# Performance work log

Hardware: AMD Instinct MI355X
Metric: run time of the kernel (lower is better)

## Reference

```python
import jax, jax.numpy as jnp
import numpy as np

B, S, D_MODEL = 1, 1024, 1024
D_CKV, D_CQ = 256, 512
N_HEAD, D_HEAD, D_ROPE = 8, 64, 32


def setup_inputs() -> dict:
    key = jax.random.key(0)
    ks = jax.random.split(key, 12)
    def w(k, shape):
        return jax.random.normal(k, shape, dtype=jnp.float32) * 0.02
    return {
        "x": jax.random.normal(ks[0], (B, S, D_MODEL), dtype=jnp.float32),
        "w_q_idx": w(ks[1], (D_MODEL, N_HEAD * D_HEAD)),
        "w_k_idx": w(ks[2], (D_MODEL, D_HEAD)),
        "w_idx": jnp.ones((N_HEAD,), dtype=jnp.float32),
        "raw_delta": jnp.zeros((D_ROPE // 2,), dtype=jnp.float32),
        "w_dkv": w(ks[3], (D_MODEL, D_CKV)),
        "w_uk": w(ks[4], (D_CKV, N_HEAD * D_HEAD)),
        "w_uv": w(ks[5], (D_CKV, N_HEAD * D_HEAD)),
        "w_dq": w(ks[6], (D_MODEL, D_CQ)),
        "w_uq": w(ks[7], (D_CQ, N_HEAD * D_HEAD)),
        "w_qr": w(ks[8], (D_CQ, N_HEAD * D_ROPE)),
        "w_kr": w(ks[9], (D_MODEL, D_ROPE)),
        "w_out": w(ks[10], (N_HEAD * D_HEAD, D_MODEL)),
        "k_ts": 128,
        "local_window": 64,
    }


def _pope(x, raw_delta, theta):
    # x: (b, L, H, d_rope); positions run along axis 1 (matches torch PoPE)
    delta = -2.0 * jnp.pi * jax.nn.sigmoid(raw_delta)            # (d2,)
    pos = jnp.arange(x.shape[1], dtype=x.dtype)
    ang = pos[None, :, None, None] * theta + delta               # (1, L, 1, d2)
    c, s = jnp.cos(ang), jnp.sin(ang)
    mu1, mu2 = jnp.split(jax.nn.softplus(x), 2, axis=-1)
    return jnp.concatenate((mu1 * c - mu2 * s, mu1 * s + mu2 * c), axis=-1)


def reference(x, w_q_idx, w_k_idx, w_idx, raw_delta, w_dkv, w_uk, w_uv,
              w_dq, w_uq, w_qr, w_kr, w_out, k_ts, local_window):
    b, s, _ = x.shape
    h, dh, dr = N_HEAD, D_HEAD, D_ROPE
    theta = 1.0 / (10000.0 ** (2.0 * jnp.arange(dr // 2, dtype=jnp.float32) / dr))

    # ---- LightningIndexer: per-head relu'd relevance, combined with learned head weights
    qI = (x @ w_q_idx).reshape(b, s, h, dh)
    kI = x @ w_k_idx                                             # (b, s, dh)
    sc = jax.nn.relu(jnp.einsum('bthd,bsd->bths', qI, kI))
    I = jnp.einsum('bths,h->bts', sc, w_idx)

    # ---- TokenSelector: force local window in, mask future out, top-k indices
    qp = jnp.arange(s)[:, None]
    kp = jnp.arange(s)[None, :]
    local = (kp >= qp - local_window + 1) & (kp <= qp)
    causal = kp > qp
    I = jnp.where(local, jnp.inf, I)
    I = jnp.where(causal, -jnp.inf, I)
    k = min(k_ts, s)
    _, idx = jax.lax.top_k(I, k)                                 # (b, s, k) int32

    gather = jax.vmap(lambda t, i: t[i])                         # (s,d),(l,k)->(l,k,d)

    # ---- MLA latent KV, gathered per query
    c_kv = x @ w_dkv                                             # (b, s, d_ckv)
    ckv_sel = gather(c_kv, idx)                                  # (b, s, k, d_ckv)
    key_c = (ckv_sel @ w_uk).reshape(b, s, k, h, dh).transpose(0, 3, 1, 2, 4)
    value = (ckv_sel @ w_uv).reshape(b, s, k, h, dh).transpose(0, 3, 1, 2, 4)

    c_q = x @ w_dq
    query_c = (c_q @ w_uq).reshape(b, s, h, dh).transpose(0, 2, 1, 3)
    query_r = _pope((c_q @ w_qr).reshape(b, s, h, dr), raw_delta, theta).transpose(0, 2, 1, 3)

    # key rope: PoPE applied with positions along the k (selected-token) axis,
    # exactly as the torch code's permute(0,2,1,3) does
    x_sel = gather(x, idx)                                       # (b, s, k, d_model)
    kr = _pope((x_sel @ w_kr).transpose(0, 2, 1, 3), raw_delta, theta).transpose(0, 2, 1, 3)
    key_r = jnp.broadcast_to(kr[:, None], (b, h, s, k, dr))

    query = jnp.concatenate((query_c, query_r), axis=-1)         # (b, h, s, dh+dr)
    keyt = jnp.concatenate((key_c, key_r), axis=-1)              # (b, h, s, k, dh+dr)
    scale = (dh + dr) ** -0.5
    scores = jnp.einsum('bhld,bhlkd->bhlk', query, keyt) * scale
    attn = jax.nn.softmax(scores, axis=-1)
    out = jnp.einsum('bhlk,bhlkd->bhld', attn, value)
    out = out.transpose(0, 2, 1, 3).reshape(b, s, h * dh)
    return out @ w_out
```

## Files before the change

kernel.cpp:

```cpp
#include <hip/hip_runtime.h>
#include <math.h>

#define S_LEN 1024
#define NH 8

typedef __attribute__((ext_vector_type(8))) short bf16x8;
typedef __attribute__((ext_vector_type(4))) float f32x4;

__device__ __forceinline__ float sp_softplus(float x) {
    return fmaxf(x, 0.f) + log1pf(expf(-fabsf(x)));
}

__device__ __forceinline__ unsigned short bfu(float f) {
    unsigned u = __float_as_uint(f);
    unsigned r = (u + 0x7FFFu + ((u >> 16) & 1u)) >> 16;
    return (unsigned short)r;
}

struct FRONT {
    const float *x, *wqidx, *wkidx, *raw_delta, *wuk;
    const float *wdkv, *wdq, *wkr, *wuq, *wqr, *wuv, *wout;
    float *qIP, *kIP, *csc, *css;
    unsigned short *wdkvT, *wdqT, *wkrT, *wuqT, *wqrT, *wuvT, *woutT, *wukb;
};

__global__ __launch_bounds__(256) void front_kernel(FRONT f)
{
    __shared__ float As[2][16][18];
    __shared__ float Bs[2][16][68];
    __shared__ unsigned short tile[64][65];
    int bx = blockIdx.x;
    if (bx < 1152) {
        int gx = bx % 18, gy = bx / 18;
        int half = threadIdx.x >> 7;
        int t = threadIdx.x & 127;
        int u = gx * 2 + half;
        const float* B; float* C;
        int ldb, N, n0, kb;
        if (u < 32) {
            B = f.wqidx; ldb = 512; N = 512;
            C = f.qIP + (long)(u >> 3) * 524288;
            n0 = (u & 7) * 64;
            kb = (u >> 3) * 256;
        } else {
            B = f.wkidx; ldb = 64; N = 64;
            C = f.kIP + (long)(u - 32) * 65536;
            n0 = 0;
            kb = (u - 32) * 256;
        }
        int ke = kb + 256;
        int m0 = gy * 16;
        int ar = t >> 2, ak = t & 3;
        int bk = t >> 3, bn = t & 7;
        int ty = t >> 4, tx = t & 15;

        float4 aN = make_float4(0.f, 0.f, 0.f, 0.f);
        if (t < 64) aN = *(const float4*)(f.x + (long)(m0 + ar) * 1024 + kb + ak * 4);
        float4 b0 = *(const float4*)(B + (long)(kb + bk) * ldb + n0 + bn * 4);
        float4 b1 = *(const float4*)(B + (long)(kb + bk) * ldb + n0 + (bn + 8) * 4);
        float acc[2][4] = {};
        for (int k0 = kb; k0 < ke; k0 += 16) {
            if (t < 64) {
                As[half][ak * 4 + 0][ar] = aN.x;
                As[half][ak * 4 + 1][ar] = aN.y;
                As[half][ak * 4 + 2][ar] = aN.z;
                As[half][ak * 4 + 3][ar] = aN.w;
            }
            *(float4*)&Bs[half][bk][bn * 4] = b0;
            *(float4*)&Bs[half][bk][(bn + 8) * 4] = b1;
            __syncthreads();
            if (k0 + 16 < ke) {
                if (t < 64) aN = *(const float4*)(f.x + (long)(m0 + ar) * 1024 + (k0 + 16) + ak * 4);
                b0 = *(const float4*)(B + (long)(k0 + 16 + bk) * ldb + n0 + bn * 4);
                b1 = *(const float4*)(B + (long)(k0 + 16 + bk) * ldb + n0 + (bn + 8) * 4);
            }
            #pragma unroll
            for (int kk = 0; kk < 16; ++kk) {
                float2 a = *(float2*)&As[half][kk][ty * 2];
                float4 b = *(float4*)&Bs[half][kk][tx * 4];
                acc[0][0] += a.x * b.x; acc[0][1] += a.x * b.y;
                acc[0][2] += a.x * b.z; acc[0][3] += a.x * b.w;
                acc[1][0] += a.y * b.x; acc[1][1] += a.y * b.y;
                acc[1][2] += a.y * b.z; acc[1][3] += a.y * b.w;
            }
            __syncthreads();
        }
        #pragma unroll
        for (int i = 0; i < 2; ++i) {
            float4 v = make_float4(acc[i][0], acc[i][1], acc[i][2], acc[i][3]);
            *(float4*)(C + (long)(m0 + ty * 2 + i) * N + n0 + tx * 4) = v;
        }
    } else if (bx < 1616) {
        int b = bx - 1152;
        const float* srcs[7] = {f.wdkv, f.wdq, f.wkr, f.wuq, f.wqr, f.wuv, f.wout};
        unsigned short* dsts[7] = {f.wdkvT, f.wdqT, f.wkrT, f.wuqT, f.wqrT, f.wuvT, f.woutT};
        const int Ns[7]   = {256, 512, 32, 512, 256, 512, 1024};
        const int Klds[7] = {1024, 1024, 1024, 512, 512, 256, 512};
        const int Ntl[7]  = {4, 8, 1, 8, 4, 8, 16};
        const int bst[8]  = {0, 64, 192, 208, 272, 304, 336, 464};
        int e = 0;
        #pragma unroll
        for (int i = 1; i < 7; ++i) if (b >= bst[i]) e = i;
        int lb = b - bst[e];
        int nt = lb % Ntl[e], kt = lb / Ntl[e];
        const float* src = srcs[e];
        unsigned short* dst = dsts[e];
        int N = Ns[e], Kld = Klds[e];
        int k0 = kt * 64, n0 = nt * 64;
        int t = threadIdx.x;
        int c = t & 63, r4 = t >> 6;
        #pragma unroll
        for (int it = 0; it < 16; ++it) {
            int r = it * 4 + r4;
            float v = (n0 + c < N) ? src[(long)(k0 + r) * N + n0 + c] : 0.f;
            tile[r][c] = bfu(v);
        }
        __syncthreads();
        int wq = t & 7;
        #pragma unroll
        for (int itw = 0; itw < 2; ++itw) {
            int wr = itw * 32 + (t >> 3);
            if (n0 + wr < N) {
                unsigned short v[8];
                #pragma unroll
                for (int j = 0; j < 8; ++j) v[j] = tile[wq * 8 + j][wr];
                *(uint4*)(dst + (long)(n0 + wr) * Kld + k0 + wq * 8) = *(uint4*)v;
            }
        }
    } else if (bx < 1624) {
        int idx = (bx - 1616) * 256 + threadIdx.x;
        int j = idx >> 4, i = idx & 15;
        float rd = f.raw_delta[i];
        float delta = -6.283185307179586f * (1.f / (1.f + expf(-rd)));
        float th = exp2f(-(float)i * 0.83048202372184f);
        float ang = (float)j * th + delta;
        float sv, cv;
        sincosf(ang, &sv, &cv);
        f.csc[idx] = cv;
        f.css[idx] = sv;
    } else {
        int idx = (bx - 1624) * 256 + threadIdx.x;
        f.wukb[idx] = bfu(f.wuk[idx]);
    }
}

struct MFG {
    const float* A[10]; const unsigned short* B[10]; float* C[10];
    int lda[10], ldb[10], ldc[10], K[10], N[10], obf[10];
    int tstart[11]; int ne;
};

__global__ __launch_bounds__(256) void mgemm(MFG mg)
{
    int bx = blockIdx.x, e = 0;
    #pragma unroll
    for (int i = 1; i < 10; ++i) if (i < mg.ne && bx >= mg.tstart[i]) e = i;
    const float* A = mg.A[e];
    const unsigned short* B = mg.B[e];
    float* C = mg.C[e];
    int lda = mg.lda[e], ldb = mg.ldb[e], ldc = mg.ldc[e];
    int K = mg.K[e], N = mg.N[e];
    int m0 = blockIdx.y * 64, n0 = (bx - mg.tstart[e]) * 64;

    __shared__ unsigned short As[64][40];
    __shared__ unsigned short Bs[64][40];
    int t = threadIdx.x;
    int srow = t >> 2, skq = t & 3;
    int wid = t >> 6, l = t & 63;
    int wm = (wid >> 1) * 32, wn = (wid & 1) * 32;
    int fr = l & 15, fk = (l >> 4) * 8;
    bool bok = (n0 + srow) < N;

    f32x4 acc00 = {0.f, 0.f, 0.f, 0.f};
    f32x4 acc01 = {0.f, 0.f, 0.f, 0.f};
    f32x4 acc10 = {0.f, 0.f, 0.f, 0.f};
    f32x4 acc11 = {0.f, 0.f, 0.f, 0.f};

    for (int k0 = 0; k0 < K; k0 += 32) {
        {
            const float* ap = A + (long)(m0 + srow) * lda + k0 + skq * 8;
            float4 v0 = *(const float4*)ap;
            float4 v1 = *(const float4*)(ap + 4);
            unsigned short* d = &As[srow][skq * 8];
            d[0] = bfu(v0.x); d[1] = bfu(v0.y); d[2] = bfu(v0.z); d[3] = bfu(v0.w);
            d[4] = bfu(v1.x); d[5] = bfu(v1.y); d[6] = bfu(v1.z); d[7] = bfu(v1.w);
        }
        {
            uint4 bv = make_uint4(0u, 0u, 0u, 0u);
            if (bok) bv = *(const uint4*)(B + (long)(n0 + srow) * ldb + k0 + skq * 8);
            *(uint4*)&Bs[srow][skq * 8] = bv;
        }
        __syncthreads();
        bf16x8 a0 = *(bf16x8*)&As[wm + fr][fk];
        bf16x8 a1 = *(bf16x8*)&As[wm + 16 + fr][fk];
        bf16x8 b0 = *(bf16x8*)&Bs[wn + fr][fk];
        bf16x8 b1 = *(bf16x8*)&Bs[wn + 16 + fr][fk];
        acc00 = __builtin_amdgcn_mfma_f32_16x16x32_bf16(a0, b0, acc00, 0, 0, 0);
        acc01 = __builtin_amdgcn_mfma_f32_16x16x32_bf16(a0, b1, acc01, 0, 0, 0);
        acc10 = __builtin_amdgcn_mfma_f32_16x16x32_bf16(a1, b0, acc10, 0, 0, 0);
        acc11 = __builtin_amdgcn_mfma_f32_16x16x32_bf16(a1, b1, acc11, 0, 0, 0);
        __syncthreads();
    }
    int crow = (l >> 4) * 4;
    int col0 = n0 + wn + fr, col1 = n0 + wn + 16 + fr;
    if (mg.obf[e]) {
        unsigned short* Cu = (unsigned short*)C;
        if (col0 < N) {
            #pragma unroll
            for (int r = 0; r < 4; ++r) {
                Cu[(long)(m0 + wm + crow + r) * ldc + col0]      = bfu(acc00[r]);
                Cu[(long)(m0 + wm + 16 + crow + r) * ldc + col0] = bfu(acc10[r]);
            }
        }
        if (col1 < N) {
            #pragma unroll
            for (int r = 0; r < 4; ++r) {
                Cu[(long)(m0 + wm + crow + r) * ldc + col1]      = bfu(acc01[r]);
                Cu[(long)(m0 + wm + 16 + crow + r) * ldc + col1] = bfu(acc11[r]);
            }
        }
    } else {
        if (col0 < N) {
            #pragma unroll
            for (int r = 0; r < 4; ++r) {
                C[(long)(m0 + wm + crow + r) * ldc + col0]      = acc00[r];
                C[(long)(m0 + wm + 16 + crow + r) * ldc + col0] = acc10[r];
            }
        }
        if (col1 < N) {
            #pragma unroll
            for (int r = 0; r < 4; ++r) {
                C[(long)(m0 + wm + crow + r) * ldc + col1]      = acc01[r];
                C[(long)(m0 + wm + 16 + crow + r) * ldc + col1] = acc11[r];
            }
        }
    }
}

struct MIDARG {
    const float *qIP, *kIP, *w_idx; float* I;
    const float* qc; const unsigned short* wukb; float* qabs;
    const float *qrp, *raw_delta; float* qrr;
    const float* xkr; float* mu;
};

__global__ __launch_bounds__(256) void mid_kernel(MIDARG g)
{
    __shared__ __align__(16) char smem[26112];
    int b = blockIdx.x;
    int t = threadIdx.x;
    if (b < 512) {
        int sb = b % 16, tb = b / 16;
        if (sb * 64 > tb * 32 + 31) return;
        int t0 = tb * 32, s0 = sb * 64;
        float (*ksT)[68] = (float(*)[68])smem;
        float (*qs)[68]  = (float(*)[68])(smem + 17408);
        {
            int r = t & 63, q = t >> 6;
            #pragma unroll
            for (int u = 0; u < 4; ++u) {
                int c4 = q * 4 + u;
                long off = (long)(s0 + r) * 64 + c4 * 4;
                float4 v = *(const float4*)(g.kIP + off);
                #pragma unroll
                for (int s = 1; s < 4; ++s) {
                    float4 v2 = *(const float4*)(g.kIP + (long)s * 65536 + off);
                    v.x += v2.x; v.y += v2.y; v.z += v2.z; v.w += v2.w;
                }
                ksT[c4 * 4 + 0][r] = v.x;
                ksT[c4 * 4 + 1][r] = v.y;
                ksT[c4 * 4 + 2][r] = v.z;
                ksT[c4 * 4 + 3][r] = v.w;
            }
        }
        int ty = t >> 4, tx = t & 15;
        float accI[2][4] = {};
        for (int h = 0; h < 8; ++h) {
            __syncthreads();
            {
                int r = t >> 3, q = t & 7;
                long base = (long)(t0 + r) * 512 + h * 64;
                #pragma unroll
                for (int half = 0; half < 2; ++half) {
                    long off = base + (q + half * 8) * 4;
                    float4 a = *(const float4*)(g.qIP + off);
                    #pragma unroll
                    for (int s = 1; s < 4; ++s) {
                        float4 a1 = *(const float4*)(g.qIP + (long)s * 524288 + off);
                        a.x += a1.x; a.y += a1.y; a.z += a1.z; a.w += a1.w;
                    }
                    *(float4*)&qs[r][(q + half * 8) * 4] = a;
                }
            }
            __syncthreads();
            float acc[2][4] = {};
            #pragma unroll
            for (int dc = 0; dc < 4; ++dc) {
                float a0[16], a1[16];
                #pragma unroll
                for (int u = 0; u < 4; ++u) {
                    float4 v0 = *(float4*)&qs[ty * 2][dc * 16 + u * 4];
                    float4 v1 = *(float4*)&qs[ty * 2 + 1][dc * 16 + u * 4];
                    a0[u * 4 + 0] = v0.x; a0[u * 4 + 1] = v0.y; a0[u * 4 + 2] = v0.z; a0[u * 4 + 3] = v0.w;
                    a1[u * 4 + 0] = v1.x; a1[u * 4 + 1] = v1.y; a1[u * 4 + 2] = v1.z; a1[u * 4 + 3] = v1.w;
                }
                #pragma unroll
                for (int kk = 0; kk < 16; ++kk) {
                    int d = dc * 16 + kk;
                    float4 bb = *(float4*)&ksT[d][tx * 4];
                    acc[0][0] += a0[kk] * bb.x; acc[0][1] += a0[kk] * bb.y;
                    acc[0][2] += a0[kk] * bb.z; acc[0][3] += a0[kk] * bb.w;
                    acc[1][0] += a1[kk] * bb.x; acc[1][1] += a1[kk] * bb.y;
                    acc[1][2] += a1[kk] * bb.z; acc[1][3] += a1[kk] * bb.w;
                }
            }
            float wh = g.w_idx[h];
            #pragma unroll
            for (int i = 0; i < 2; ++i)
                #pragma unroll
                for (int j = 0; j < 4; ++j)
                    accI[i][j] += wh * fmaxf(acc[i][j], 0.f);
        }
        #pragma unroll
        for (int i = 0; i < 2; ++i) {
            float4 v = make_float4(accI[i][0], accI[i][1], accI[i][2], accI[i][3]);
            *(float4*)&g.I[(long)(t0 + ty * 2 + i) * 1024 + s0 + tx * 4] = v;
        }
    } else if (b < 1024) {
        int lb = b - 512;
        int h = lb >> 6, rem = lb & 63;
        int n0 = (rem >> 4) * 64, m0 = (rem & 15) * 64;
        const float* A = g.qc + h * 64;
        const unsigned short* B = g.wukb + h * 64;
        float* C = g.qabs + h * 256;
        unsigned short (*As)[40] = (unsigned short(*)[40])smem;
        unsigned short (*Bs)[40] = (unsigned short(*)[40])(smem + 5120);
        int srow = t >> 2, skq = t & 3;
        int wid = t >> 6, l = t & 63;
        int wm = (wid >> 1) * 32, wn = (wid & 1) * 32;
        int fr = l & 15, fk = (l >> 4) * 8;
        f32x4 acc00 = {0.f, 0.f, 0.f, 0.f};
        f32x4 acc01 = {0.f, 0.f, 0.f, 0.f};
        f32x4 acc10 = {0.f, 0.f, 0.f, 0.f};
        f32x4 acc11 = {0.f, 0.f, 0.f, 0.f};
        for (int k0 = 0; k0 < 64; k0 += 32) {
            {
                const float* ap = A + (long)(m0 + srow) * 512 + k0 + skq * 8;
                float4 v0 = *(const float4*)ap;
                float4 v1 = *(const float4*)(ap + 4);
                unsigned short* d = &As[srow][skq * 8];
                d[0] = bfu(v0.x); d[1] = bfu(v0.y); d[2] = bfu(v0.z); d[3] = bfu(v0.w);
                d[4] = bfu(v1.x); d[5] = bfu(v1.y); d[6] = bfu(v1.z); d[7] = bfu(v1.w);
            }
            {
                uint4 bv = *(const uint4*)(B + (long)(n0 + srow) * 512 + k0 + skq * 8);
                *(uint4*)&Bs[srow][skq * 8] = bv;
            }
            __syncthreads();
            bf16x8 a0 = *(bf16x8*)&As[wm + fr][fk];
            bf16x8 a1 = *(bf16x8*)&As[wm + 16 + fr][fk];
            bf16x8 b0 = *(bf16x8*)&Bs[wn + fr][fk];
            bf16x8 b1 = *(bf16x8*)&Bs[wn + 16 + fr][fk];
            acc00 = __builtin_amdgcn_mfma_f32_16x16x32_bf16(a0, b0, acc00, 0, 0, 0);
            acc01 = __builtin_amdgcn_mfma_f32_16x16x32_bf16(a0, b1, acc01, 0, 0, 0);
            acc10 = __builtin_amdgcn_mfma_f32_16x16x32_bf16(a1, b0, acc10, 0, 0, 0);
            acc11 = __builtin_amdgcn_mfma_f32_16x16x32_bf16(a1, b1, acc11, 0, 0, 0);
            __syncthreads();
        }
        int crow = (l >> 4) * 4;
        int col0 = n0 + wn + fr, col1 = n0 + wn + 16 + fr;
        #pragma unroll
        for (int r = 0; r < 4; ++r) {
            C[(long)(m0 + wm + crow + r) * 2048 + col0]      = acc00[r];
            C[(long)(m0 + wm + 16 + crow + r) * 2048 + col0] = acc10[r];
            C[(long)(m0 + wm + crow + r) * 2048 + col1]      = acc01[r];
            C[(long)(m0 + wm + 16 + crow + r) * 2048 + col1] = acc11[r];
        }
    } else if (b < 1536) {
        int tq = (b - 1024) * 2 + (t >> 7);
        int tt = t & 127;
        int h = tt >> 4, i = tt & 15;
        float rd = g.raw_delta[i];
        float delta = -6.283185307179586f * (1.f / (1.f + expf(-rd)));
        float th = exp2f(-(float)i * 0.83048202372184f);
        float ang = (float)tq * th + delta;
        float sv, cv;
        sincosf(ang, &sv, &cv);
        float m1 = sp_softplus(g.qrp[tq * 256 + h * 32 + i]);
        float m2 = sp_softplus(g.qrp[tq * 256 + h * 32 + 16 + i]);
        g.qrr[tq * 256 + h * 32 + i]      = m1 * cv - m2 * sv;
        g.qrr[tq * 256 + h * 32 + 16 + i] = m1 * sv + m2 * cv;
    } else {
        int i = (b - 1536) * 256 + t;
        g.mu[i] = sp_softplus(g.xkr[i]);
    }
}

__global__ __launch_bounds__(256) void topk_kernel(
    const float* __restrict__ I, int* __restrict__ idxout)
{
    int t = blockIdx.x * 4 + (threadIdx.x >> 6);
    int lane = threadIdx.x & 63;
    int smin = max(0, t - 63);
    int w = min(64, t + 1);
    if (lane < w) idxout[t * 128 + lane] = smin + lane;
    for (int q = t + 1 + lane; q < 128; q += 64)
        idxout[t * 128 + q] = q;
    int f = max(0, t - 63);
    int m = min(f, 64);
    if (m == 0) return;
    const float* row = I + (long)t * 1024;

    unsigned long long key[16];
    #pragma unroll
    for (int g4 = 0; g4 < 4; ++g4) {
        float4 v = *(const float4*)(row + lane * 16 + g4 * 4);
        float vv[4] = {v.x, v.y, v.z, v.w};
        #pragma unroll
        for (int j = 0; j < 4; ++j) {
            int s = lane * 16 + g4 * 4 + j;
            unsigned long long k = 0ull;
            if (s < f) {
                unsigned u = __float_as_uint(vv[j]);
                unsigned ou = (u & 0x80000000u) ? ~u : (u | 0x80000000u);
                k = ((unsigned long long)ou << 32) | (0xFFFFFFFFu - (unsigned)s);
            }
            key[g4 * 4 + j] = k;
        }
    }

    #pragma unroll
    for (int km = 1; km <= 10; ++km) {
        #pragma unroll
        for (int jm = km - 1; jm >= 0; --jm) {
            if (jm >= 4) {
                int lmask = 1 << (jm - 4);
                #pragma unroll
                for (int r = 0; r < 16; ++r) {
                    unsigned long long other = __shfl_xor(key[r], lmask, 64);
                    int i = lane * 16 + r;
                    bool keep_max = (((i & (1 << km)) == 0) == ((i & (1 << jm)) == 0));
                    unsigned long long mx = key[r] > other ? key[r] : other;
                    unsigned long long mn = key[r] > other ? other : key[r];
                    key[r] = keep_max ? mx : mn;
                }
            } else {
                int rmask = 1 << jm;
                #pragma unroll
                for (int r = 0; r < 16; ++r) {
                    if ((r & rmask) == 0) {
                        int r2 = r | rmask;
                        int i = lane * 16 + r;
                        bool keep_max_low = ((i & (1 << km)) == 0);
                        unsigned long long a = key[r], b = key[r2];
                        unsigned long long mx = a > b ? a : b;
                        unsigned long long mn = a > b ? b : a;
                        key[r]  = keep_max_low ? mx : mn;
                        key[r2] = keep_max_low ? mn : mx;
                    }
                }
            }
        }
    }

    if (lane < 4) {
        #pragma unroll
        for (int r = 0; r < 16; ++r) {
            int e = lane * 16 + r;
            if (e < m) {
                int s = (int)(0xFFFFFFFFu - (unsigned)(key[r] & 0xFFFFFFFFull));
                idxout[t * 128 + w + e] = s;
            }
        }
    }
}

__global__ __launch_bounds__(256) void attn_kernel(
    const float* __restrict__ qabs, const float* __restrict__ qrr,
    const unsigned short* __restrict__ ckvb, const float* __restrict__ mu,
    const float* __restrict__ csc, const float* __restrict__ css,
    const int* __restrict__ idxb, float* __restrict__ olat)
{
    __shared__ unsigned short kv[64][296];
    __shared__ float sc[8][68];
    __shared__ float hs[16];
    __shared__ int idx_s[128];

    int t = blockIdx.x, tid = threadIdx.x;
    int w = tid >> 6, l = tid & 63;
    const float scale = 0.10206207261596575f;

    if (tid < 128) idx_s[tid] = idxb[t * 128 + tid];
    {
        int r = tid >> 5;
        for (int c = tid & 31; c < 296; c += 32) {
            float v = 0.f;
            if (c < 256)      v = qabs[(long)t * 2048 + r * 256 + c] * scale;
            else if (c < 288) v = qrr[(long)t * 256 + r * 32 + (c - 256)] * scale;
            kv[r][c] = bfu(v);
            kv[r + 8][c] = 0;
        }
    }
    __syncthreads();

    bf16x8 qf[9];
    #pragma unroll
    for (int ks = 0; ks < 9; ++ks)
        qf[ks] = *(bf16x8*)&kv[l & 15][ks * 32 + (l >> 4) * 8];

    float mrun0 = -INFINITY, mrun1 = -INFINITY;
    float lrun0 = 0.f, lrun1 = 0.f;
    float acc0 = 0, acc1 = 0, acc2 = 0, acc3 = 0;
    float acc4 = 0, acc5 = 0, acc6 = 0, acc7 = 0;

    int sr = tid >> 2, sq = tid & 3;
    int hpv = l >> 3;
    int c8 = w * 64 + (l & 7) * 8;

    #pragma unroll
    for (int chunk = 0; chunk < 2; ++chunk) {
        __syncthreads();
        {
            int src = idx_s[chunk * 64 + sr];
            const uint4* sp = (const uint4*)(ckvb + (long)src * 256) + sq * 8;
            uint4* dp = (uint4*)&kv[sr][0] + sq * 8;
            #pragma unroll
            for (int g = 0; g < 8; ++g) dp[g] = sp[g];
        }
        {
            int src = idx_s[chunk * 64 + sr];
            int j = chunk * 64 + sr;
            unsigned short hh[8];
            #pragma unroll
            for (int ii = 0; ii < 8; ++ii) {
                int i = sq * 8 + ii;
                int i15 = i & 15;
                float m1 = mu[src * 32 + i15];
                float m2 = mu[src * 32 + 16 + i15];
                float cv = csc[j * 16 + i15];
                float sv = css[j * 16 + i15];
                float kr = (i < 16) ? (m1 * cv - m2 * sv) : (m1 * sv + m2 * cv);
                hh[ii] = bfu(kr);
            }
            *(uint4*)&kv[sr][256 + sq * 8] = *(uint4*)hh;
        }
        __syncthreads();

        f32x4 st = {0.f, 0.f, 0.f, 0.f};
        #pragma unroll
        for (int ks = 0; ks < 9; ++ks) {
            bf16x8 af = *(bf16x8*)&kv[w * 16 + (l & 15)][ks * 32 + (l >> 4) * 8];
            st = __builtin_amdgcn_mfma_f32_16x16x32_bf16(af, qf[ks], st, 0, 0, 0);
        }
        {
            int hcol = l & 15;
            int srow2 = w * 16 + (l >> 4) * 4;
            if (hcol < 8) {
                #pragma unroll
                for (int r = 0; r < 4; ++r) sc[hcol][srow2 + r] = st[r];
            }
        }
        __syncthreads();

        float rh0, rh1;
        {
            int h = 2 * w;
            float v = sc[h][l];
            float mx = v;
            #pragma unroll
            for (int off = 32; off > 0; off >>= 1) mx = fmaxf(mx, __shfl_xor(mx, off));
            float mnew = fmaxf(mrun0, mx);
            float p = expf(v - mnew);
            float ps = p;
            #pragma unroll
            for (int off = 32; off > 0; off >>= 1) ps += __shfl_xor(ps, off);
            rh0 = expf(mrun0 - mnew);
            lrun0 = lrun0 * rh0 + ps;
            mrun0 = mnew;
            sc[h][l] = p;
        }
        {
            int h = 2 * w + 1;
            float v = sc[h][l];
            float mx = v;
            #pragma unroll
            for (int off = 32; off > 0; off >>= 1) mx = fmaxf(mx, __shfl_xor(mx, off));
            float mnew = fmaxf(mrun1, mx);
            float p = expf(v - mnew);
            float ps = p;
            #pragma unroll
            for (int off = 32; off > 0; off >>= 1) ps += __shfl_xor(ps, off);
            rh1 = expf(mrun1 - mnew);
            lrun1 = lrun1 * rh1 + ps;
            mrun1 = mnew;
            sc[h][l] = p;
        }
        if (l == 0) {
            hs[2 * w] = rh0;
            hs[2 * w + 1] = rh1;
            if (chunk == 1) {
                hs[8 + 2 * w] = lrun0;
                hs[8 + 2 * w + 1] = lrun1;
            }
        }
        __syncthreads();

        float rsel = hs[hpv];
        acc0 *= rsel; acc1 *= rsel; acc2 *= rsel; acc3 *= rsel;
        acc4 *= rsel; acc5 *= rsel; acc6 *= rsel; acc7 *= rsel;
        #pragma unroll 4
        for (int j = 0; j < 64; ++j) {
            float p = sc[hpv][j];
            uint4 vv = *(uint4*)&kv[j][c8];
            acc0 += p * __uint_as_float(vv.x << 16);
            acc1 += p * __uint_as_float(vv.x & 0xffff0000u);
            acc2 += p * __uint_as_float(vv.y << 16);
            acc3 += p * __uint_as_float(vv.y & 0xffff0000u);
            acc4 += p * __uint_as_float(vv.z << 16);
            acc5 += p * __uint_as_float(vv.z & 0xffff0000u);
            acc6 += p * __uint_as_float(vv.w << 16);
            acc7 += p * __uint_as_float(vv.w & 0xffff0000u);
        }
    }

    float inv = 1.f / hs[8 + hpv];
    float* op = olat + (long)t * 2048 + hpv * 256 + c8;
    *(float4*)op       = make_float4(acc0 * inv, acc1 * inv, acc2 * inv, acc3 * inv);
    *(float4*)(op + 4) = make_float4(acc4 * inv, acc5 * inv, acc6 * inv, acc7 * inv);
}

extern "C" void kernel_launch(void* const* d_in, const int* in_sizes, int n_in,
                              void* d_out, int out_size, void* d_ws, size_t ws_size,
                              hipStream_t stream)
{
    const float* x         = (const float*)d_in[0];
    const float* w_q_idx   = (const float*)d_in[1];
    const float* w_k_idx   = (const float*)d_in[2];
    const float* w_idx     = (const float*)d_in[3];
    const float* raw_delta = (const float*)d_in[4];
    const float* w_dkv     = (const float*)d_in[5];
    const float* w_uk      = (const float*)d_in[6];
    const float* w_uv      = (const float*)d_in[7];
    const float* w_dq      = (const float*)d_in[8];
    const float* w_uq      = (const float*)d_in[9];
    const float* w_qr      = (const float*)d_in[10];
    const float* w_kr      = (const float*)d_in[11];
    const float* w_out     = (const float*)d_in[12];
    (void)in_sizes; (void)n_in; (void)out_size; (void)ws_size;
    float* out = (float*)d_out;

    float* ws = (float*)d_ws;
    unsigned short* ckvb = (unsigned short*)ws;   ws += 131072;
    float* cq    = ws;        ws += 1024 * 512;
    float* xkr   = ws;        ws += 1024 * 32;
    float* qrp   = ws;        ws += 1024 * 256;
    float* qrr   = ws;        ws += 1024 * 256;
    float* qc    = ws;        ws += 1024 * 512;
    float* qabs  = ws;        ws += 1024 * 2048;
    float* Ibuf  = ws;        ws += 1024 * 1024;
    int*   idxb  = (int*)ws;  ws += 1024 * 128;
    float* olat  = ws;        ws += 1024 * 2048;
    float* outh  = ws;        ws += 1024 * 512;
    float* mu    = ws;        ws += 1024 * 32;
    float* cscb  = ws;        ws += 128 * 16;
    float* cssb  = ws;        ws += 128 * 16;
    unsigned short* wdkvT = (unsigned short*)ws;  ws += 131072;
    unsigned short* wdqT  = (unsigned short*)ws;  ws += 262144;
    unsigned short* wkrT  = (unsigned short*)ws;  ws += 16384;
    unsigned short* wuqT  = (unsigned short*)ws;  ws += 131072;
    unsigned short* wqrT  = (unsigned short*)ws;  ws += 65536;
    unsigned short* wuvT  = (unsigned short*)ws;  ws += 65536;
    unsigned short* woutT = (unsigned short*)ws;  ws += 262144;
    unsigned short* wukb  = (unsigned short*)ws;  ws += 65536;
    float* part  = ws;        ws += 2359296;
    float* qIP = part;
    float* kIP = part + 2097152;

    {
        FRONT f{};
        f.x = x; f.wqidx = w_q_idx; f.wkidx = w_k_idx; f.raw_delta = raw_delta; f.wuk = w_uk;
        f.wdkv = w_dkv; f.wdq = w_dq; f.wkr = w_kr; f.wuq = w_uq; f.wqr = w_qr;
        f.wuv = w_uv; f.wout = w_out;
        f.qIP = qIP; f.kIP = kIP; f.csc = cscb; f.css = cssb;
        f.wdkvT = wdkvT; f.wdqT = wdqT; f.wkrT = wkrT; f.wuqT = wuqT;
        f.wqrT = wqrT; f.wuvT = wuvT; f.woutT = woutT; f.wukb = wukb;
        front_kernel<<<dim3(2136), dim3(256), 0, stream>>>(f);
    }

    {
        MFG m{};
        for (int i = 0; i < 3; ++i) { m.A[i]=x; m.lda[i]=1024; m.K[i]=1024; }
        m.B[0]=wdkvT; m.C[0]=(float*)ckvb; m.ldb[0]=1024; m.ldc[0]=256; m.N[0]=256; m.obf[0]=1;
        m.B[1]=wdqT;  m.C[1]=cq;           m.ldb[1]=1024; m.ldc[1]=512; m.N[1]=512;
        m.B[2]=wkrT;  m.C[2]=xkr;          m.ldb[2]=1024; m.ldc[2]=32;  m.N[2]=32;
        m.tstart[0]=0; m.tstart[1]=4; m.tstart[2]=12; m.tstart[3]=13;
        m.ne = 3;
        mgemm<<<dim3(13, 16), dim3(256), 0, stream>>>(m);
    }

    {
        MFG m{};
        for (int i = 0; i < 2; ++i) { m.A[i]=cq; m.lda[i]=512; m.K[i]=512; }
        m.B[0]=wuqT; m.C[0]=qc;  m.ldb[0]=512; m.ldc[0]=512; m.N[0]=512;
        m.B[1]=wqrT; m.C[1]=qrp; m.ldb[1]=512; m.ldc[1]=256; m.N[1]=256;
        m.tstart[0]=0; m.tstart[1]=8; m.tstart[2]=12;
        m.ne = 2;
        mgemm<<<dim3(12, 16), dim3(256), 0, stream>>>(m);
    }

    {
        MIDARG g{};
        g.qIP = qIP; g.kIP = kIP; g.w_idx = w_idx; g.I = Ibuf;
        g.qc = qc; g.wukb = wukb; g.qabs = qabs;
        g.qrp = qrp; g.raw_delta = raw_delta; g.qrr = qrr;
        g.xkr = xkr; g.mu = mu;
        mid_kernel<<<dim3(1664), dim3(256), 0, stream>>>(g);
    }

    topk_kernel<<<dim3(256), dim3(256), 0, stream>>>(Ibuf, idxb);

    attn_kernel<<<dim3(1024), dim3(256), 0, stream>>>(qabs, qrr, ckvb, mu, cscb, cssb, idxb, olat);

    {
        MFG m{};
        for (int h = 0; h < 8; ++h) {
            m.A[h] = olat + h * 256;      m.lda[h] = 2048; m.K[h] = 256;
            m.B[h] = wuvT + h * 64 * 256; m.ldb[h] = 256;
            m.C[h] = outh + h * 64;       m.ldc[h] = 512;  m.N[h] = 64;
            m.tstart[h] = h;
        }
        m.tstart[8] = 8;
        m.ne = 8;
        mgemm<<<dim3(8, 16), dim3(256), 0, stream>>>(m);
    }

    {
        MFG m{};
        m.A[0] = outh;  m.lda[0] = 512; m.K[0] = 512;
        m.B[0] = woutT; m.ldb[0] = 512;
        m.C[0] = out;   m.ldc[0] = 1024; m.N[0] = 1024;
        m.tstart[0] = 0; m.tstart[1] = 16;
        m.ne = 1;
        mgemm<<<dim3(16, 16), dim3(256), 0, stream>>>(m);
    }
}
```

Baseline: 194.8 us.

## Read gathered KV rows and queries directly from global memory instead of LDS staging

Removes the 64x296 bf16 shared-memory tile in the attention kernel. MFMA operands for keys and queries are now loaded straight from global memory (query converted to bf16 per k-step), the rope key part is computed per lane in registers, and the PV loop reads value rows from global through the index list. This drops LDS traffic, several barriers and the shared-memory footprint, which could raise occupancy. In exchange it repeats global/L2 reads for the same rows and the same query conversion across waves, and adds more scattered global loads in the inner PV loop.

```diff
diff --git a/kernel.cpp b/kernel.cpp
--- a/kernel.cpp
+++ b/kernel.cpp
@@ -481,7 +481,6 @@
     const float* __restrict__ csc, const float* __restrict__ css,
     const int* __restrict__ idxb, float* __restrict__ olat)
 {
-    __shared__ unsigned short kv[64][296];
     __shared__ float sc[8][68];
     __shared__ float hs[16];
     __shared__ int idx_s[128];
@@ -491,73 +490,84 @@
     const float scale = 0.10206207261596575f;
 
     if (tid < 128) idx_s[tid] = idxb[t * 128 + tid];
-    {
-        int r = tid >> 5;
-        for (int c = tid & 31; c < 296; c += 32) {
-            float v = 0.f;
-            if (c < 256)      v = qabs[(long)t * 2048 + r * 256 + c] * scale;
-            else if (c < 288) v = qrr[(long)t * 256 + r * 32 + (c - 256)] * scale;
-            kv[r][c] = bfu(v);
-            kv[r + 8][c] = 0;
-        }
-    }
-    __syncthreads();
-
-    bf16x8 qf[9];
-    #pragma unroll
-    for (int ks = 0; ks < 9; ++ks)
-        qf[ks] = *(bf16x8*)&kv[l & 15][ks * 32 + (l >> 4) * 8];
+
+    int hrow = l & 15;
+    int kslice = (l >> 4) * 8;
+    int hpv = l >> 3;
+    int c8 = w * 64 + (l & 7) * 8;
 
     float mrun0 = -INFINITY, mrun1 = -INFINITY;
     float lrun0 = 0.f, lrun1 = 0.f;
     float acc0 = 0, acc1 = 0, acc2 = 0, acc3 = 0;
     float acc4 = 0, acc5 = 0, acc6 = 0, acc7 = 0;
 
-    int sr = tid >> 2, sq = tid & 3;
-    int hpv = l >> 3;
-    int c8 = w * 64 + (l & 7) * 8;
+    __syncthreads();
 
     #pragma unroll
     for (int chunk = 0; chunk < 2; ++chunk) {
-        __syncthreads();
+        if (chunk) __syncthreads();
+
+        int r = w * 16 + hrow;
+        int src = idx_s[chunk * 64 + r];
+        int jglob = chunk * 64 + r;
+        f32x4 st = {0.f, 0.f, 0.f, 0.f};
+        #pragma unroll 1
+        for (int ks = 0; ks < 8; ++ks) {
+            bf16x8 af = *(const bf16x8*)(ckvb + (long)src * 256 + ks * 32 + kslice);
+            bf16x8 qf = {0, 0, 0, 0, 0, 0, 0, 0};
+            if (hrow < 8) {
+                const float* qp = qabs + (long)t * 2048 + hrow * 256 + ks * 32 + kslice;
+                float4 a = *(const float4*)qp;
+                float4 b = *(const float4*)(qp + 4);
+                unsigned short qq[8];
+                qq[0] = bfu(a.x * scale); qq[1] = bfu(a.y * scale);
+                qq[2] = bfu(a.z * scale); qq[3] = bfu(a.w * scale);
+                qq[4] = bfu(b.x * scale); qq[5] = bfu(b.y * scale);
+                qq[6] = bfu(b.z * scale); qq[7] = bfu(b.w * scale);
+                qf = *(bf16x8*)qq;
+            }
+            st = __builtin_amdgcn_mfma_f32_16x16x32_bf16(af, qf, st, 0, 0, 0);
+        }
         {
-            int src = idx_s[chunk * 64 + sr];
-            const uint4* sp = (const uint4*)(ckvb + (long)src * 256) + sq * 8;
-            uint4* dp = (uint4*)&kv[sr][0] + sq * 8;
-            #pragma unroll
-            for (int g = 0; g < 8; ++g) dp[g] = sp[g];
+            int i15 = kslice & 15;
+            bool lo = kslice < 16;
+            float4 m1a = *(const float4*)(mu + src * 32 + i15);
+            float4 m1b = *(const float4*)(mu + src * 32 + i15 + 4);
+            float4 m2a = *(const float4*)(mu + src * 32 + 16 + i15);
+            float4 m2b = *(const float4*)(mu + src * 32 + 16 + i15 + 4);
+            float4 ca = *(const float4*)(csc + jglob * 16 + i15);
+            float4 cb = *(const float4*)(csc + jglob * 16 + i15 + 4);
+            float4 sa = *(const float4*)(css + jglob * 16 + i15);
+            float4 sb = *(const float4*)(css + jglob * 16 + i15 + 4);
+            unsigned short hh[8];
+            hh[0] = bfu(lo ? m1a.x * ca.x - m2a.x * sa.x : m1a.x * sa.x + m2a.x * ca.x);
+            hh[1] = bfu(lo ? m1a.y * ca.y - m2a.y * sa.y : m1a.y * sa.y + m2a.y * ca.y);
+            hh[2] = bfu(lo ? m1a.z * ca.z - m2a.z * sa.z : m1a.z * sa.z + m2a.z * ca.z);
+            hh[3] = bfu(lo ? m1a.w * ca.w - m2a.w * sa.w : m1a.w * sa.w + m2a.w * ca.w);
+            hh[4] = bfu(lo ? m1b.x * cb.x - m2b.x * sb.x : m1b.x * sb.x + m2b.x * cb.x);
+            hh[5] = bfu(lo ? m1b.y * cb.y - m2b.y * sb.y : m1b.y * sb.y + m2b.y * cb.y);
+            hh[6] = bfu(lo ? m1b.z * cb.z - m2b.z * sb.z : m1b.z * sb.z + m2b.z * cb.z);
+            hh[7] = bfu(lo ? m1b.w * cb.w - m2b.w * sb.w : m1b.w * sb.w + m2b.w * cb.w);
+            bf16x8 af = *(bf16x8*)hh;
+            bf16x8 qf = {0, 0, 0, 0, 0, 0, 0, 0};
+            if (hrow < 8) {
+                const float* qp = qrr + (long)t * 256 + hrow * 32 + kslice;
+                float4 a = *(const float4*)qp;
+                float4 b = *(const float4*)(qp + 4);
+                unsigned short qq[8];
+                qq[0] = bfu(a.x * scale); qq[1] = bfu(a.y * scale);
+                qq[2] = bfu(a.z * scale); qq[3] = bfu(a.w * scale);
+                qq[4] = bfu(b.x * scale); qq[5] = bfu(b.y * scale);
+                qq[6] = bfu(b.z * scale); qq[7] = bfu(b.w * scale);
+                qf = *(bf16x8*)qq;
+            }
+            st = __builtin_amdgcn_mfma_f32_16x16x32_bf16(af, qf, st, 0, 0, 0);
         }
         {
-            int src = idx_s[chunk * 64 + sr];
-            int j = chunk * 64 + sr;
-            unsigned short hh[8];
-            #pragma unroll
-            for (int ii = 0; ii < 8; ++ii) {
-                int i = sq * 8 + ii;
-                int i15 = i & 15;
-                float m1 = mu[src * 32 + i15];
-                float m2 = mu[src * 32 + 16 + i15];
-                float cv = csc[j * 16 + i15];
-                float sv = css[j * 16 + i15];
-                float kr = (i < 16) ? (m1 * cv - m2 * sv) : (m1 * sv + m2 * cv);
-                hh[ii] = bfu(kr);
-            }
-            *(uint4*)&kv[sr][256 + sq * 8] = *(uint4*)hh;
-        }
-        __syncthreads();
-
-        f32x4 st = {0.f, 0.f, 0.f, 0.f};
-        #pragma unroll
-        for (int ks = 0; ks < 9; ++ks) {
-            bf16x8 af = *(bf16x8*)&kv[w * 16 + (l & 15)][ks * 32 + (l >> 4) * 8];
-            st = __builtin_amdgcn_mfma_f32_16x16x32_bf16(af, qf[ks], st, 0, 0, 0);
-        }
-        {
-            int hcol = l & 15;
             int srow2 = w * 16 + (l >> 4) * 4;
-            if (hcol < 8) {
-                #pragma unroll
-                for (int r = 0; r < 4; ++r) sc[hcol][srow2 + r] = st[r];
+            if (hrow < 8) {
+                #pragma unroll
+                for (int rr = 0; rr < 4; ++rr) sc[hrow][srow2 + rr] = st[rr];
             }
         }
         __syncthreads();
@@ -611,7 +621,8 @@
         #pragma unroll 4
         for (int j = 0; j < 64; ++j) {
             float p = sc[hpv][j];
-            uint4 vv = *(uint4*)&kv[j][c8];
+            int srcj = idx_s[chunk * 64 + j];
+            uint4 vv = *(const uint4*)(ckvb + (long)srcj * 256 + c8);
             acc0 += p * __uint_as_float(vv.x << 16);
             acc1 += p * __uint_as_float(vv.x & 0xffff0000u);
             acc2 += p * __uint_as_float(vv.y << 16);
```

Result: no change. 193.8 us (-0.5%).
